# Performance work log

Hardware: AMD Instinct MI355X
Metric: run time of the kernel (lower is better)

Reference implementation:

```python
import jax, jax.numpy as jnp
import numpy as np

B = 16384      # batch of samples
D = 65         # inps columns: 64 input spins + 1 output spin y
NA = 64        # auxiliary (threshold) spins
N = D + NA     # spins entering vspin expansion: 129
M = N + N * (N - 1) // 2  # degree-<=2 spin monomials: 8385
GAMMA = 1.0

# pairwise index pattern (i < j), computed once at trace time
_II, _JJ = np.triu_indices(N, k=1)


def batch_vspin(b):
    # b: [B, N] -> [B, N + N(N-1)/2]: linear terms then all pairwise products b_i*b_j (i<j)
    return jnp.concatenate([b, b[:, _II] * b[:, _JJ]], axis=-1)


def setup_inputs() -> dict:
    key = jax.random.key(0)
    k1, k2, k3, k4 = jax.random.split(key, 4)
    inps = jax.random.normal(k1, (B, D), dtype=jnp.float32)
    thresh_w = jax.random.normal(k2, (NA, D), dtype=jnp.float32) * 0.1
    thresh_b = jax.random.normal(k3, (NA,), dtype=jnp.float32) * 0.1
    main_w = jax.random.normal(k4, (1, M), dtype=jnp.float32) * 0.02
    return {"inps": inps, "thresh_w": thresh_w, "thresh_b": thresh_b, "main_w": main_w}


def reference(inps, thresh_w, thresh_b, main_w):
    inps = inps.astype(jnp.float32)
    x = inps[:, :-1]                      # [B, D-1]
    y = inps[:, -1:]                      # [B, 1]
    i_right = jnp.concatenate([x, y], axis=-1)    # [B, D]
    i_wrong = jnp.concatenate([x, -y], axis=-1)   # [B, D]

    w1 = i_right @ thresh_w.T + thresh_b          # [B, NA]
    w2 = i_wrong @ thresh_w.T + thresh_b          # [B, NA]
    t1 = jnp.tanh(GAMMA * w1)
    t2 = jnp.tanh(GAMMA * w2)

    b1 = jnp.concatenate([i_right, t1], axis=-1)  # [B, N]
    b2 = jnp.concatenate([i_wrong, t2], axis=-1)  # [B, N]
    v1 = batch_vspin(b1)                          # [B, M]
    v2 = batch_vspin(b2)                          # [B, M]

    diff = (v1 - v2) @ main_w.T + 1.0             # [B, 1]
    int_penalty = jnp.sum((GAMMA / 300.0) * ((1.0 - t1 ** 2) ** 2 + (1.0 - t2 ** 2) ** 2))
    neut_penalty = jnp.sum((t2 * w2 - t1 * w1) ** 2)
    return (diff, int_penalty, neut_penalty)
```

## Files before the change

kernel.cpp:

```cpp
#include <hip/hip_runtime.h>

#define B_SZ 16384
#define N_SP 129
#define GRID 1024
#define BLOCK 256

typedef _Float16 half8 __attribute__((ext_vector_type(8)));
typedef float float4v __attribute__((ext_vector_type(4)));

__device__ float g_p1[GRID];
__device__ float g_p2[GRID];

__device__ __forceinline__ int qidx(int i, int j) {
  return N_SP + i * (2 * N_SP - i - 1) / 2 + (j - i - 1);
}

__device__ __forceinline__ float fast_tanh(float x) {
  float xc = fminf(fmaxf(x, -15.f), 15.f);
  float e = __expf(2.f * xc);
  return 1.f - 2.f / (e + 1.f);
}

__global__ __launch_bounds__(BLOCK, 4) void main_kernel(
    const float* __restrict__ inps, const float* __restrict__ tw,
    const float* __restrict__ tb, const float* __restrict__ mw,
    float* __restrict__ out) {
  __shared__ __align__(16) _Float16 s_x[1152];
  __shared__ __align__(16) _Float16 s_dt[1152];
  __shared__ float s_part[64];
  __shared__ float s_red[8];

  const int tid = threadIdx.x;
  const int l = tid & 63, wib = tid >> 6;
  const int b0 = blockIdx.x << 4;
  const int q = l >> 4, m = l & 15;
  const int u = (wib << 4) + m;

  {
    const float4* src4 = (const float4*)(inps + b0 * 65);
    float4 v = src4[tid];
#pragma unroll
    for (int c = 0; c < 4; c++) {
      unsigned idx = tid * 4 + c;
      unsigned row = idx / 65u, col = idx - row * 65u;
      s_x[row * 72 + col] = (_Float16)((const float*)&v)[c];
    }
    if (tid < 4) {
      float4 v2 = src4[256 + tid];
#pragma unroll
      for (int c = 0; c < 4; c++) {
        unsigned idx = (256 + tid) * 4 + c;
        unsigned row = idx / 65u, col = idx - row * 65u;
        s_x[row * 72 + col] = (_Float16)((const float*)&v2)[c];
      }
    }
  }

  half8 bf0, bf1, bf2, bf3, bf4, bf5;
  {
    const int k0 = q * 8;
    const int k1 = 32 + q * 8;
    const int tw_base = u * 65;
    const int q1_base = qidx(u, 65);
#pragma unroll
    for (int j = 0; j < 8; j++) bf0[j] = (_Float16)tw[tw_base + k0 + j];
#pragma unroll
    for (int j = 0; j < 8; j++) bf1[j] = (_Float16)tw[tw_base + k1 + j];
#pragma unroll
    for (int j = 0; j < 8; j++) bf2[j] = (_Float16)mw[q1_base + k0 + j];
#pragma unroll
    for (int j = 0; j < 8; j++) bf3[j] = (_Float16)mw[q1_base + k1 + j];
#pragma unroll
    for (int j = 0; j < 8; j++) {
      int k = k0 + j;
      int a = u < k ? u : k, b = u < k ? k : u;
      int idx = (u == k) ? 0 : qidx(65 + a, 65 + b);
      float v = mw[idx];
      bf4[j] = (_Float16)((u == k) ? 0.f : v);
    }
#pragma unroll
    for (int j = 0; j < 8; j++) {
      int k = k1 + j;
      int a = u < k ? u : k, b = u < k ? k : u;
      int idx = (u == k) ? 0 : qidx(65 + a, 65 + b);
      float v = mw[idx];
      bf5[j] = (_Float16)((u == k) ? 0.f : v);
    }
  }

  const float twyv = tw[u * 65 + 64];
  const float qxyv = mw[qidx(u, 64)];
  const float qytv = mw[qidx(64, 65 + u)];
  const float lintv = mw[65 + u];
  const float liny = mw[64];
  const float tbv = tb[u];

  __syncthreads();

  half8 ax0 = *(const half8*)(s_x + m * 72 + q * 8);
  half8 ax1 = *(const half8*)(s_x + m * 72 + 32 + q * 8);

  float4v acc = {0.f, 0.f, 0.f, 0.f};
  acc = __builtin_amdgcn_mfma_f32_16x16x32_f16(ax0, bf0, acc, 0, 0, 0);
  acc = __builtin_amdgcn_mfma_f32_16x16x32_f16(ax1, bf1, acc, 0, 0, 0);

  float yv[4], dtv[4], stv[4];
  float pint = 0.f, pneut = 0.f;
#pragma unroll
  for (int r = 0; r < 4; r++) {
    yv[r] = (float)s_x[(q * 4 + r) * 72 + 64];
    float wpre = acc[r] + tbv;
    float w1 = wpre + twyv * yv[r];
    float w2 = wpre - twyv * yv[r];
    float t1 = fast_tanh(w1), t2 = fast_tanh(w2);
    dtv[r] = t1 - t2; stv[r] = t1 + t2;
    float a1 = 1.f - t1 * t1, a2 = 1.f - t2 * t2;
    pint += a1 * a1 + a2 * a2;
    float nv = t2 * w2 - t1 * w1;
    pneut += nv * nv;
    s_dt[(q * 4 + r) * 72 + u] = (_Float16)dtv[r];
  }
  __syncthreads();

  half8 ad0 = *(const half8*)(s_dt + m * 72 + q * 8);
  half8 ad1 = *(const half8*)(s_dt + m * 72 + 32 + q * 8);

  float4v rxt = {0.f, 0.f, 0.f, 0.f}, rtt = {0.f, 0.f, 0.f, 0.f};
  rxt = __builtin_amdgcn_mfma_f32_16x16x32_f16(ad0, bf2, rxt, 0, 0, 0);
  rxt = __builtin_amdgcn_mfma_f32_16x16x32_f16(ad1, bf3, rxt, 0, 0, 0);
  rtt = __builtin_amdgcn_mfma_f32_16x16x32_f16(ad0, bf4, rtt, 0, 0, 0);
  rtt = __builtin_amdgcn_mfma_f32_16x16x32_f16(ad1, bf5, rtt, 0, 0, 0);

  float creg[4];
#pragma unroll
  for (int r = 0; r < 4; r++) {
    float xv = (float)s_x[(q * 4 + r) * 72 + u];
    float c = xv * (2.f * yv[r] * qxyv + rxt[r])
            + yv[r] * stv[r] * qytv
            + 0.5f * stv[r] * rtt[r]
            + lintv * dtv[r];
    c += __shfl_xor(c, 1); c += __shfl_xor(c, 2);
    c += __shfl_xor(c, 4); c += __shfl_xor(c, 8);
    creg[r] = c;
  }
  if (m == 0) {
#pragma unroll
    for (int r = 0; r < 4; r++) s_part[wib * 16 + q * 4 + r] = creg[r];
  }

#pragma unroll
  for (int off = 1; off < 64; off <<= 1) {
    pint += __shfl_xor(pint, off);
    pneut += __shfl_xor(pneut, off);
  }
  if (l == 0) { s_red[wib] = pint; s_red[4 + wib] = pneut; }
  __syncthreads();

  if (tid < 16) {
    float c = s_part[tid] + s_part[16 + tid] + s_part[32 + tid] + s_part[48 + tid];
    float y = (float)s_x[tid * 72 + 64];
    out[b0 + tid] = 1.f + 2.f * y * liny + c;
  }
  if (tid == 0) {
    g_p1[blockIdx.x] = s_red[0] + s_red[1] + s_red[2] + s_red[3];
    g_p2[blockIdx.x] = s_red[4] + s_red[5] + s_red[6] + s_red[7];
  }
}

__global__ __launch_bounds__(1024) void reduce_kernel(float* __restrict__ out) {
  __shared__ float s[32];
  const int tid = threadIdx.x;
  float a = g_p1[tid];
  float b = g_p2[tid];
#pragma unroll
  for (int off = 1; off < 64; off <<= 1) {
    a += __shfl_xor(a, off);
    b += __shfl_xor(b, off);
  }
  const int w = tid >> 6, l = tid & 63;
  if (l == 0) { s[w] = a; s[16 + w] = b; }
  __syncthreads();
  if (tid == 0) {
    float sa = 0.f, sb = 0.f;
#pragma unroll
    for (int i = 0; i < 16; i++) { sa += s[i]; sb += s[16 + i]; }
    out[B_SZ] = sa * (1.f / 300.f);
    out[B_SZ + 1] = sb;
  }
}

extern "C" void kernel_launch(void* const* d_in, const int* in_sizes, int n_in,
                              void* d_out, int out_size, void* d_ws, size_t ws_size,
                              hipStream_t stream) {
  const float* inps = (const float*)d_in[0];
  const float* tw   = (const float*)d_in[1];
  const float* tb   = (const float*)d_in[2];
  const float* mw   = (const float*)d_in[3];
  float* out = (float*)d_out;
  (void)d_ws; (void)ws_size;
  main_kernel<<<GRID, BLOCK, 0, stream>>>(inps, tw, tb, mw, out);
  reduce_kernel<<<1, 1024, 0, stream>>>(out);
}
```

Before: 71.73 us.

## Stage weight matrices in shared memory via coalesced cooperative loads

Replaces per-thread scattered global gathers of thresh_w and the quadratic main_w blocks with block-wide coalesced loads into three fp16 shared-memory tiles. The aux-aux pair block is unpacked from its triangular layout with a sqrt-based index inversion and mirrored symmetrically. MFMA B-operands are then read as half8 vectors from LDS. This targets the cost of uncoalesced, index-heavy global loads, but it adds about 27KB of LDS per block, which may lower occupancy, and each block still reloads the full weight set.

```diff
diff --git a/kernel.cpp b/kernel.cpp
--- a/kernel.cpp
+++ b/kernel.cpp
@@ -25,6 +25,9 @@
     const float* __restrict__ inps, const float* __restrict__ tw,
     const float* __restrict__ tb, const float* __restrict__ mw,
     float* __restrict__ out) {
+  __shared__ __align__(16) _Float16 s_tw[64 * 72];
+  __shared__ __align__(16) _Float16 s_qxt[64 * 72];
+  __shared__ __align__(16) _Float16 s_qtt[64 * 72];
   __shared__ __align__(16) _Float16 s_x[1152];
   __shared__ __align__(16) _Float16 s_dt[1152];
   __shared__ float s_part[64];
@@ -56,36 +59,61 @@
     }
   }
 
-  half8 bf0, bf1, bf2, bf3, bf4, bf5;
-  {
-    const int k0 = q * 8;
-    const int k1 = 32 + q * 8;
-    const int tw_base = u * 65;
-    const int q1_base = qidx(u, 65);
-#pragma unroll
-    for (int j = 0; j < 8; j++) bf0[j] = (_Float16)tw[tw_base + k0 + j];
-#pragma unroll
-    for (int j = 0; j < 8; j++) bf1[j] = (_Float16)tw[tw_base + k1 + j];
-#pragma unroll
-    for (int j = 0; j < 8; j++) bf2[j] = (_Float16)mw[q1_base + k0 + j];
-#pragma unroll
-    for (int j = 0; j < 8; j++) bf3[j] = (_Float16)mw[q1_base + k1 + j];
-#pragma unroll
-    for (int j = 0; j < 8; j++) {
-      int k = k0 + j;
-      int a = u < k ? u : k, b = u < k ? k : u;
-      int idx = (u == k) ? 0 : qidx(65 + a, 65 + b);
-      float v = mw[idx];
-      bf4[j] = (_Float16)((u == k) ? 0.f : v);
-    }
-#pragma unroll
-    for (int j = 0; j < 8; j++) {
-      int k = k1 + j;
-      int a = u < k ? u : k, b = u < k ? k : u;
-      int idx = (u == k) ? 0 : qidx(65 + a, 65 + b);
-      float v = mw[idx];
-      bf5[j] = (_Float16)((u == k) ? 0.f : v);
-    }
+  {
+    const float4* src4 = (const float4*)tw;
+#pragma unroll
+    for (int s = 0; s < 4; s++) {
+      float4 v = src4[tid + 256 * s];
+#pragma unroll
+      for (int c = 0; c < 4; c++) {
+        unsigned idx = (tid + 256 * s) * 4 + c;
+        unsigned row = idx / 65u, col = idx - row * 65u;
+        s_tw[row * 72 + col] = (_Float16)((const float*)&v)[c];
+      }
+    }
+    if (tid < 16) {
+      float4 v = src4[1024 + tid];
+#pragma unroll
+      for (int c = 0; c < 4; c++) {
+        unsigned idx = (1024 + tid) * 4 + c;
+        unsigned row = idx / 65u, col = idx - row * 65u;
+        s_tw[row * 72 + col] = (_Float16)((const float*)&v)[c];
+      }
+    }
+  }
+
+  {
+#pragma unroll
+    for (int s = 0; s < 16; s++) {
+      int d = tid + 256 * s;
+      int i = d >> 6, k = d & 63;
+      int src = 193 + ((i * (257 - i)) >> 1) - i + k;
+      s_qxt[i * 72 + k] = (_Float16)mw[src];
+    }
+  }
+
+  {
+    if (tid < 252) {
+      const float* srcp = mw + 6369 + tid * 8;
+      float v[8];
+#pragma unroll
+      for (int e = 0; e < 8; e++) v[e] = srcp[e];
+      int p0 = tid * 8;
+      int a = (int)((127.0f - sqrtf((float)(16129 - 8 * p0))) * 0.5f);
+      if (a < 0) a = 0;
+      if (a > 62) a = 62;
+      while (a > 0 && (a * (127 - a)) / 2 > p0) --a;
+      while (a < 62 && ((a + 1) * (126 - a)) / 2 <= p0) ++a;
+      int b = a + 1 + (p0 - (a * (127 - a)) / 2);
+#pragma unroll
+      for (int e = 0; e < 8; e++) {
+        _Float16 h = (_Float16)v[e];
+        s_qtt[a * 72 + b] = h;
+        s_qtt[b * 72 + a] = h;
+        if (++b > 63) { ++a; b = a + 1; }
+      }
+    }
+    if (tid < 64) s_qtt[tid * 72 + tid] = (_Float16)0.f;
   }
 
   const float twyv = tw[u * 65 + 64];
@@ -99,10 +127,12 @@
 
   half8 ax0 = *(const half8*)(s_x + m * 72 + q * 8);
   half8 ax1 = *(const half8*)(s_x + m * 72 + 32 + q * 8);
+  half8 bt0 = *(const half8*)(s_tw + u * 72 + q * 8);
+  half8 bt1 = *(const half8*)(s_tw + u * 72 + 32 + q * 8);
 
   float4v acc = {0.f, 0.f, 0.f, 0.f};
-  acc = __builtin_amdgcn_mfma_f32_16x16x32_f16(ax0, bf0, acc, 0, 0, 0);
-  acc = __builtin_amdgcn_mfma_f32_16x16x32_f16(ax1, bf1, acc, 0, 0, 0);
+  acc = __builtin_amdgcn_mfma_f32_16x16x32_f16(ax0, bt0, acc, 0, 0, 0);
+  acc = __builtin_amdgcn_mfma_f32_16x16x32_f16(ax1, bt1, acc, 0, 0, 0);
 
   float yv[4], dtv[4], stv[4];
   float pint = 0.f, pneut = 0.f;
@@ -124,12 +154,16 @@
 
   half8 ad0 = *(const half8*)(s_dt + m * 72 + q * 8);
   half8 ad1 = *(const half8*)(s_dt + m * 72 + 32 + q * 8);
+  half8 bq0 = *(const half8*)(s_qxt + u * 72 + q * 8);
+  half8 bq1 = *(const half8*)(s_qxt + u * 72 + 32 + q * 8);
+  half8 bs0 = *(const half8*)(s_qtt + u * 72 + q * 8);
+  half8 bs1 = *(const half8*)(s_qtt + u * 72 + 32 + q * 8);
 
   float4v rxt = {0.f, 0.f, 0.f, 0.f}, rtt = {0.f, 0.f, 0.f, 0.f};
-  rxt = __builtin_amdgcn_mfma_f32_16x16x32_f16(ad0, bf2, rxt, 0, 0, 0);
-  rxt = __builtin_amdgcn_mfma_f32_16x16x32_f16(ad1, bf3, rxt, 0, 0, 0);
-  rtt = __builtin_amdgcn_mfma_f32_16x16x32_f16(ad0, bf4, rtt, 0, 0, 0);
-  rtt = __builtin_amdgcn_mfma_f32_16x16x32_f16(ad1, bf5, rtt, 0, 0, 0);
+  rxt = __builtin_amdgcn_mfma_f32_16x16x32_f16(ad0, bq0, rxt, 0, 0, 0);
+  rxt = __builtin_amdgcn_mfma_f32_16x16x32_f16(ad1, bq1, rxt, 0, 0, 0);
+  rtt = __builtin_amdgcn_mfma_f32_16x16x32_f16(ad0, bs0, rtt, 0, 0, 0);
+  rtt = __builtin_amdgcn_mfma_f32_16x16x32_f16(ad1, bs1, rtt, 0, 0, 0);
 
   float creg[4];
 #pragma unroll
```

Measured after the change: 71.36 us. About the same (-0.5%).
